# Kernel optimization log

Hardware: AMD Instinct MI355X
Metric: run time of the kernel (lower is better)

The kernel has to match this reference:

```python
import jax, jax.numpy as jnp
import numpy as np

N = 150_000   # total nodes in batched graph
E = 900_000   # total edges (avg in-degree ~ 2*n_gram = 6)
D = 300       # hidden_size_node (GloVe 300d)
B = 512       # number of graphs (docs) in batch
C = 20        # class_num
SLOPE = 0.01  # torch LeakyReLU default negative_slope


def _lrelu(x):
    return jnp.where(x >= 0, x, SLOPE * x)


def setup_inputs() -> dict:
    key = jax.random.key(0)
    ks = jax.random.split(key, 8)
    node_h = jax.random.normal(ks[0], (N, D), dtype=jnp.float32)
    eta = jax.random.uniform(ks[1], (N, 1), dtype=jnp.float32)
    W_attn = jax.random.normal(ks[2], (2 * D, 1), dtype=jnp.float32) * 0.05
    b_attn = jnp.zeros((1,), dtype=jnp.float32)
    W_lin = jax.random.normal(ks[3], (D, C), dtype=jnp.float32) * 0.05
    b_lin = jnp.zeros((C,), dtype=jnp.float32)
    src = jax.random.randint(ks[4], (E,), 0, N, dtype=jnp.int32)
    dst = jax.random.randint(ks[5], (E,), 0, N, dtype=jnp.int32)
    graph_ids = jnp.sort(jax.random.randint(ks[6], (N,), 0, B, dtype=jnp.int32))
    return {
        "node_h": node_h, "eta": eta,
        "W_attn": W_attn, "b_attn": b_attn,
        "W_lin": W_lin, "b_lin": b_lin,
        "src": src, "dst": dst,
        "graph_ids": graph_ids, "num_graphs": B,
    }


def reference(node_h, eta, W_attn, b_attn, W_lin, b_lin, src, dst, graph_ids, num_graphs):
    n = node_h.shape[0]
    # edge_attention: leaky_relu(attn_fc(cat(h_src, h_dst))).
    # cat@W == h_src@W[:D] + h_dst@W[D:], so project per-node first (avoids [E,2D] cat).
    ps = node_h @ W_attn[:D]          # [N,1]
    pd = node_h @ W_attn[D:]          # [N,1]
    w = _lrelu(ps[src] + pd[dst] + b_attn)   # [E,1] edge scores

    # segment softmax over each destination node's mailbox
    deg = jax.ops.segment_sum(jnp.ones((w.shape[0], 1), w.dtype), dst, num_segments=n)  # [N,1]
    wmax = jax.ops.segment_max(w, dst, num_segments=n)
    wmax = jnp.where(deg > 0, wmax, 0.0)     # neutralize -inf for isolated nodes
    ew = jnp.exp(w - wmax[dst])              # [E,1]
    denom = jax.ops.segment_sum(ew, dst, num_segments=n)
    a = ew / jnp.where(denom[dst] > 0, denom[dst], 1.0)   # [E,1] softmax weights

    # gcn_reduce: max over weighted messages a * h_src per destination
    am = a * node_h[src]                      # [E,D]
    agg = jax.ops.segment_max(am, dst, num_segments=n)    # [N,D]
    agg = jnp.where(deg > 0, agg, 0.0)

    # gated update: eta*h + (1-eta)*agg; DGL leaves message-less nodes untouched
    h_new = eta * node_h + (1.0 - eta) * agg
    h_new = jnp.where(deg > 0, h_new, node_h)

    # dgl.sum_nodes per graph, dropout (eval: identity), leaky_relu, classifier
    hg = jax.ops.segment_sum(h_new, graph_ids, num_segments=num_graphs)  # [B,D]
    return _lrelu(hg) @ W_lin + b_lin        # [B,C]
```

## Files before the change

kernel.cpp:

```cpp
#include <hip/hip_runtime.h>
#include <math.h>


#define SLOPE 0.01f
#define KNODES 8
#define MAXT 192

__device__ __forceinline__ float lrelu(float x) { return x >= 0.f ? x : SLOPE * x; }

__device__ __forceinline__ float wrsum(float v) {
#pragma unroll
    for (int m = 32; m >= 1; m >>= 1) v += __shfl_xor(v, m, 64);
    return v;
}
__device__ __forceinline__ float wrmax(float v) {
#pragma unroll
    for (int m = 32; m >= 1; m >>= 1) v = fmaxf(v, __shfl_xor(v, m, 64));
    return v;
}

__device__ __forceinline__ void compute_bpre(const unsigned* __restrict__ bsum,
                                             int nT, unsigned* lb) {
    if (threadIdx.x < 64) {
        int l = threadIdx.x;
        unsigned a0 = (3 * l     < nT) ? bsum[3 * l]     : 0u;
        unsigned a1 = (3 * l + 1 < nT) ? bsum[3 * l + 1] : 0u;
        unsigned a2 = (3 * l + 2 < nT) ? bsum[3 * l + 2] : 0u;
        unsigned tot = a0 + a1 + a2, x = tot;
#pragma unroll
        for (int d = 1; d < 64; d <<= 1) {
            unsigned y = __shfl_up(x, d, 64);
            if (l >= d) x += y;
        }
        unsigned excl = x - tot;
        if (3 * l     < nT) lb[3 * l]     = excl;
        if (3 * l + 1 < nT) lb[3 * l + 1] = excl + a0;
        if (3 * l + 2 < nT) lb[3 * l + 2] = excl + a0 + a1;
    }
    __syncthreads();
}

__global__ __launch_bounds__(256) void k_prep(
    const float* __restrict__ H, const float* __restrict__ Wa,
    const int* __restrict__ dst,
    float* __restrict__ ps, float* __restrict__ pd,
    unsigned* __restrict__ deg,
    unsigned* __restrict__ zbase, size_t zn,
    int N, int D, int E, int nb_ps, int nb_hist) {
    int b = blockIdx.x;
    if (b < nb_ps) {
        int wid  = b * 4 + (threadIdx.x >> 6);
        int lane = threadIdx.x & 63;
        if (wid >= N) return;
        const float4* row = (const float4*)(H + (size_t)wid * D);
        const float4* wa0 = (const float4*)Wa;
        const float4* wa1 = (const float4*)(Wa + D);
        int nv = D >> 2;
        float s0 = 0.f, s1 = 0.f;
        for (int v = lane; v < nv; v += 64) {
            float4 h = row[v], a = wa0[v], c = wa1[v];
            s0 += h.x * a.x + h.y * a.y + h.z * a.z + h.w * a.w;
            s1 += h.x * c.x + h.y * c.y + h.z * c.z + h.w * c.w;
        }
        s0 = wrsum(s0);
        s1 = wrsum(s1);
        if (lane == 0) { ps[wid] = s0; pd[wid] = s1; }
    } else if (b < nb_ps + nb_hist) {
        int e = (b - nb_ps) * 256 + threadIdx.x;
        if (e < E) atomicAdd(&deg[dst[e]], 1u);
    } else {
        int    nbz    = gridDim.x - nb_ps - nb_hist;
        size_t i      = (size_t)(b - nb_ps - nb_hist) * 256 + threadIdx.x;
        size_t stride = (size_t)nbz * 256;
        for (; i < zn; i += stride) zbase[i] = 0u;
    }
}

__global__ __launch_bounds__(256) void k_scan1(
    const unsigned* __restrict__ deg, unsigned* __restrict__ loffs,
    unsigned* __restrict__ bsum, int N) {
    __shared__ unsigned wsum[4];
    int t = threadIdx.x, b = blockIdx.x;
    int base = b * 1024 + t * 4;
    unsigned v[4];
#pragma unroll
    for (int j = 0; j < 4; j++) { int i = base + j; v[j] = (i < N) ? deg[i] : 0u; }
    unsigned p0 = v[0], p1 = p0 + v[1], p2 = p1 + v[2];
    unsigned tot = p2 + v[3];
    unsigned x = tot;
    int lane = t & 63, w = t >> 6;
#pragma unroll
    for (int d = 1; d < 64; d <<= 1) { unsigned y = __shfl_up(x, d, 64); if (lane >= d) x += y; }
    if (lane == 63) wsum[w] = x;
    __syncthreads();
    unsigned woff = 0;
    for (int i = 0; i < w; i++) woff += wsum[i];
    unsigned excl = woff + x - tot;
    unsigned o[4] = {excl, excl + p0, excl + p1, excl + p2};
#pragma unroll
    for (int j = 0; j < 4; j++) { int i = base + j; if (i < N) loffs[i] = o[j]; }
    if (t == 255) bsum[b] = excl + tot;
}

__global__ __launch_bounds__(256) void k_scatter(
    const int* __restrict__ src, const int* __restrict__ dst,
    const unsigned* __restrict__ loffs, const unsigned* __restrict__ bsum,
    unsigned* __restrict__ cur, int* __restrict__ ssrc, int E, int nT) {
    __shared__ unsigned lb[MAXT];
    compute_bpre(bsum, nT, lb);
    int e = blockIdx.x * 256 + threadIdx.x;
    if (e >= E) return;
    int d = dst[e];
    unsigned base = loffs[d] + lb[d >> 10];
    unsigned r = atomicAdd(&cur[d], 1u);
    ssrc[base + r] = src[e];
}

__global__ __launch_bounds__(256) void k_fused(
    const float* __restrict__ H, const float* __restrict__ eta,
    const float* __restrict__ ps, const float* __restrict__ pd,
    const float* __restrict__ battn,
    const unsigned* __restrict__ loffs, const unsigned* __restrict__ bsum,
    const int* __restrict__ ssrc, const int* __restrict__ gid,
    float* __restrict__ hg, int N, int D, int E, int nT) {
    __shared__ unsigned lb[MAXT];
    compute_bpre(bsum, nT, lb);

    int wid  = (blockIdx.x * blockDim.x + threadIdx.x) >> 6;
    int lane = threadIdx.x & 63;
    int n0 = wid * KNODES;
    if (n0 >= N) return;
    int n1 = min(n0 + KNODES, N);
    int nv = D >> 2;
    bool q0 = lane < nv;
    bool q1 = (64 + lane) < nv;
    float b0 = battn[0];

    float sx = 0.f, sy = 0.f, sz = 0.f, sw = 0.f;
    float tx = 0.f, ty = 0.f, tz = 0.f, tw = 0.f;
    int curg = gid[n0];

    for (int n = n0; n < n1; ++n) {
        unsigned e0 = loffs[n] + lb[n >> 10];
        unsigned e1 = (n + 1 < N) ? (loffs[n + 1] + lb[(n + 1) >> 10]) : (unsigned)E;
        int degn = (int)(e1 - e0);
        const float4* hrow = (const float4*)(H + (size_t)n * D);
        float4 h0 = {0, 0, 0, 0}, h1 = {0, 0, 0, 0};
        if (q0) h0 = hrow[lane];
        if (q1) h1 = hrow[64 + lane];
        float hx = h0.x, hy = h0.y, hz = h0.z, hw = h0.w;
        float gx = h1.x, gy = h1.y, gz = h1.z, gw = h1.w;
        if (degn > 0) {
            float pdn = pd[n] + b0;
            float ax = -INFINITY, ay = -INFINITY, az = -INFINITY, aw = -INFINITY;
            float bx = -INFINITY, by = -INFINITY, bz = -INFINITY, bw = -INFINITY;
            if (degn <= 64) {
                int   sn_l = (lane < degn) ? ssrc[e0 + lane] : 0;
                float w_l  = (lane < degn) ? lrelu(ps[sn_l] + pdn) : -INFINITY;
                float m    = wrmax(w_l);
                float ex   = (lane < degn) ? expf(w_l - m) : 0.f;
                float s    = wrsum(ex);
                float a_l  = ex * (1.f / s);
                int e = 0;
                for (; e + 3 < degn; e += 4) {
                    float a0s = __shfl(a_l, e, 64),     a1s = __shfl(a_l, e + 1, 64);
                    float a2s = __shfl(a_l, e + 2, 64), a3s = __shfl(a_l, e + 3, 64);
                    int   s0i = __shfl(sn_l, e, 64),     s1i = __shfl(sn_l, e + 1, 64);
                    int   s2i = __shfl(sn_l, e + 2, 64), s3i = __shfl(sn_l, e + 3, 64);
                    const float4* r0 = (const float4*)(H + (size_t)s0i * D);
                    const float4* r1 = (const float4*)(H + (size_t)s1i * D);
                    const float4* r2 = (const float4*)(H + (size_t)s2i * D);
                    const float4* r3 = (const float4*)(H + (size_t)s3i * D);
                    if (q0) {
                        float4 u0 = r0[lane], u1 = r1[lane], u2 = r2[lane], u3 = r3[lane];
                        ax = fmaxf(fmaxf(fmaxf(ax, a0s * u0.x), a1s * u1.x), fmaxf(a2s * u2.x, a3s * u3.x));
                        ay = fmaxf(fmaxf(fmaxf(ay, a0s * u0.y), a1s * u1.y), fmaxf(a2s * u2.y, a3s * u3.y));
                        az = fmaxf(fmaxf(fmaxf(az, a0s * u0.z), a1s * u1.z), fmaxf(a2s * u2.z, a3s * u3.z));
                        aw = fmaxf(fmaxf(fmaxf(aw, a0s * u0.w), a1s * u1.w), fmaxf(a2s * u2.w, a3s * u3.w));
                    }
                    if (q1) {
                        float4 u0 = r0[64 + lane], u1 = r1[64 + lane], u2 = r2[64 + lane], u3 = r3[64 + lane];
                        bx = fmaxf(fmaxf(fmaxf(bx, a0s * u0.x), a1s * u1.x), fmaxf(a2s * u2.x, a3s * u3.x));
                        by = fmaxf(fmaxf(fmaxf(by, a0s * u0.y), a1s * u1.y), fmaxf(a2s * u2.y, a3s * u3.y));
                        bz = fmaxf(fmaxf(fmaxf(bz, a0s * u0.z), a1s * u1.z), fmaxf(a2s * u2.z, a3s * u3.z));
                        bw = fmaxf(fmaxf(fmaxf(bw, a0s * u0.w), a1s * u1.w), fmaxf(a2s * u2.w, a3s * u3.w));
                    }
                }
                for (; e + 1 < degn; e += 2) {
                    float a0s = __shfl(a_l, e, 64), a1s = __shfl(a_l, e + 1, 64);
                    int   s0i = __shfl(sn_l, e, 64), s1i = __shfl(sn_l, e + 1, 64);
                    const float4* r0 = (const float4*)(H + (size_t)s0i * D);
                    const float4* r1 = (const float4*)(H + (size_t)s1i * D);
                    if (q0) {
                        float4 u0 = r0[lane], u1 = r1[lane];
                        ax = fmaxf(fmaxf(ax, a0s * u0.x), a1s * u1.x);
                        ay = fmaxf(fmaxf(ay, a0s * u0.y), a1s * u1.y);
                        az = fmaxf(fmaxf(az, a0s * u0.z), a1s * u1.z);
                        aw = fmaxf(fmaxf(aw, a0s * u0.w), a1s * u1.w);
                    }
                    if (q1) {
                        float4 u0 = r0[64 + lane], u1 = r1[64 + lane];
                        bx = fmaxf(fmaxf(bx, a0s * u0.x), a1s * u1.x);
                        by = fmaxf(fmaxf(by, a0s * u0.y), a1s * u1.y);
                        bz = fmaxf(fmaxf(bz, a0s * u0.z), a1s * u1.z);
                        bw = fmaxf(fmaxf(bw, a0s * u0.w), a1s * u1.w);
                    }
                }
                if (e < degn) {
                    float a  = __shfl(a_l, e, 64);
                    int   sn = __shfl(sn_l, e, 64);
                    const float4* srow = (const float4*)(H + (size_t)sn * D);
                    if (q0) {
                        float4 v0 = srow[lane];
                        ax = fmaxf(ax, a * v0.x); ay = fmaxf(ay, a * v0.y);
                        az = fmaxf(az, a * v0.z); aw = fmaxf(aw, a * v0.w);
                    }
                    if (q1) {
                        float4 v1 = srow[64 + lane];
                        bx = fmaxf(bx, a * v1.x); by = fmaxf(by, a * v1.y);
                        bz = fmaxf(bz, a * v1.z); bw = fmaxf(bw, a * v1.w);
                    }
                }
            } else {
                float mm = -INFINITY;
                for (unsigned e = e0 + lane; e < e1; e += 64)
                    mm = fmaxf(mm, lrelu(ps[ssrc[e]] + pdn));
                float m = wrmax(mm);
                float ssum = 0.f;
                for (unsigned e = e0 + lane; e < e1; e += 64)
                    ssum += expf(lrelu(ps[ssrc[e]] + pdn) - m);
                float s = wrsum(ssum), inv = 1.f / s;
                for (unsigned e = e0; e < e1; ++e) {
                    int sn = ssrc[e];
                    float a = expf(lrelu(ps[sn] + pdn) - m) * inv;
                    const float4* srow = (const float4*)(H + (size_t)sn * D);
                    if (q0) {
                        float4 v0 = srow[lane];
                        ax = fmaxf(ax, a * v0.x); ay = fmaxf(ay, a * v0.y);
                        az = fmaxf(az, a * v0.z); aw = fmaxf(aw, a * v0.w);
                    }
                    if (q1) {
                        float4 v1 = srow[64 + lane];
                        bx = fmaxf(bx, a * v1.x); by = fmaxf(by, a * v1.y);
                        bz = fmaxf(bz, a * v1.z); bw = fmaxf(bw, a * v1.w);
                    }
                }
            }
            float et = eta[n], om = 1.f - et;
            hx = et * h0.x + om * ax; hy = et * h0.y + om * ay;
            hz = et * h0.z + om * az; hw = et * h0.w + om * aw;
            gx = et * h1.x + om * bx; gy = et * h1.y + om * by;
            gz = et * h1.z + om * bz; gw = et * h1.w + om * bw;
        }
        int g = gid[n];
        if (g != curg) {
            float* row = hg + (size_t)curg * D;
            int c = 4 * lane;
            if (q0) {
                atomicAdd(&row[c + 0], sx); atomicAdd(&row[c + 1], sy);
                atomicAdd(&row[c + 2], sz); atomicAdd(&row[c + 3], sw);
            }
            if (q1) {
                int c1 = 4 * (64 + lane);
                atomicAdd(&row[c1 + 0], tx); atomicAdd(&row[c1 + 1], ty);
                atomicAdd(&row[c1 + 2], tz); atomicAdd(&row[c1 + 3], tw);
            }
            sx = sy = sz = sw = tx = ty = tz = tw = 0.f;
            curg = g;
        }
        sx += hx; sy += hy; sz += hz; sw += hw;
        if (q1) { tx += gx; ty += gy; tz += gz; tw += gw; }
    }
    float* row = hg + (size_t)curg * D;
    int c = 4 * lane;
    if (q0) {
        atomicAdd(&row[c + 0], sx); atomicAdd(&row[c + 1], sy);
        atomicAdd(&row[c + 2], sz); atomicAdd(&row[c + 3], sw);
    }
    if (q1) {
        int c1 = 4 * (64 + lane);
        atomicAdd(&row[c1 + 0], tx); atomicAdd(&row[c1 + 1], ty);
        atomicAdd(&row[c1 + 2], tz); atomicAdd(&row[c1 + 3], tw);
    }
}

__global__ __launch_bounds__(64) void k_out(
    const float* __restrict__ hg, const float* __restrict__ Wl,
    const float* __restrict__ bl, float* __restrict__ out,
    int D, int C) {
    int b = blockIdx.x;
    int c = threadIdx.x;
    if (c >= C) return;
    const float* row = hg + (size_t)b * D;
    float acc = 0.f;
    for (int d = 0; d < D; ++d)
        acc += lrelu(row[d]) * Wl[(size_t)d * C + c];
    out[(size_t)b * C + c] = acc + bl[c];
}

extern "C" void kernel_launch(void* const* d_in, const int* in_sizes, int n_in,
                              void* d_out, int out_size, void* d_ws, size_t ws_size,
                              hipStream_t stream) {
    const float* H   = (const float*)d_in[0];
    const float* eta = (const float*)d_in[1];
    const float* Wa  = (const float*)d_in[2];
    const float* ba  = (const float*)d_in[3];
    const float* Wl  = (const float*)d_in[4];
    const float* bl  = (const float*)d_in[5];
    const int*   src = (const int*)d_in[6];
    const int*   dst = (const int*)d_in[7];
    const int*   gid = (const int*)d_in[8];

    const int N = in_sizes[1];
    const int D = in_sizes[2] / 2;
    const int C = in_sizes[5];
    const int E = in_sizes[6];
    const int B = out_size / C;

    char* w = (char*)d_ws;
    float*    ps    = (float*)w;    w += (size_t)N * 4;
    float*    pd    = (float*)w;    w += (size_t)N * 4;
    unsigned* deg   = (unsigned*)w; w += (size_t)N * 4;
    unsigned* cur   = (unsigned*)w; w += (size_t)N * 4;
    float*    hg    = (float*)w;    w += (size_t)B * D * 4;
    unsigned* loffs = (unsigned*)w; w += (size_t)N * 4;
    unsigned* bsum  = (unsigned*)w; w += 256 * 4;
    int*      ssrc  = (int*)w;      w += (size_t)E * 4;

    hipMemsetAsync(deg, 0, (size_t)N * 4, stream);

    const int nT      = (N + 1023) / 1024;
    const int nb_ps   = (N + 3) / 4;
    const int nb_hist = (E + 255) / 256;
    const int nb_zero = 256;
    const size_t zn   = (size_t)N + (size_t)B * D;

    k_prep<<<dim3(nb_ps + nb_hist + nb_zero), dim3(256), 0, stream>>>(
        H, Wa, dst, ps, pd, deg, cur, zn, N, D, E, nb_ps, nb_hist);
    k_scan1<<<dim3(nT), dim3(256), 0, stream>>>(deg, loffs, bsum, N);
    k_scatter<<<dim3((E + 255) / 256), dim3(256), 0, stream>>>(
        src, dst, loffs, bsum, cur, ssrc, E, nT);
    {
        int waves  = (N + KNODES - 1) / KNODES;
        int blocks = (waves + 3) / 4;
        k_fused<<<dim3(blocks), dim3(256), 0, stream>>>(
            H, eta, ps, pd, ba, loffs, bsum, ssrc, gid, hg, N, D, E, nT);
    }
    k_out<<<dim3(B), dim3(64), 0, stream>>>(hg, Wl, bl, (float*)d_out, D, C);
}
```

Measured before the change: 688.1 us.

## Record edge rank during degree histogram, drop second atomic pass and zeroing blocks

The degree histogram now stores each edge's atomic return value as its rank, so the scatter kernel writes directly to the sorted slot without a second atomic counter array. Zeroing of hg moves into one memset that covers deg and hg together (they are now contiguous), replacing the zeroing blocks inside k_prep. The 4-edge unrolled gather loop in the fused kernel is removed, leaving only the 2-edge loop, and k_out splits the D reduction across four waves. This adds an E-sized rank buffer write and read, in exchange for removing E atomics and the cur array.

```diff
diff --git a/kernel.cpp b/kernel.cpp
--- a/kernel.cpp
+++ b/kernel.cpp
@@ -44,9 +44,8 @@
     const float* __restrict__ H, const float* __restrict__ Wa,
     const int* __restrict__ dst,
     float* __restrict__ ps, float* __restrict__ pd,
-    unsigned* __restrict__ deg,
-    unsigned* __restrict__ zbase, size_t zn,
-    int N, int D, int E, int nb_ps, int nb_hist) {
+    unsigned* __restrict__ deg, unsigned* __restrict__ erank,
+    int N, int D, int E, int nb_ps) {
     int b = blockIdx.x;
     if (b < nb_ps) {
         int wid  = b * 4 + (threadIdx.x >> 6);
@@ -65,14 +64,9 @@
         s0 = wrsum(s0);
         s1 = wrsum(s1);
         if (lane == 0) { ps[wid] = s0; pd[wid] = s1; }
-    } else if (b < nb_ps + nb_hist) {
+    } else {
         int e = (b - nb_ps) * 256 + threadIdx.x;
-        if (e < E) atomicAdd(&deg[dst[e]], 1u);
-    } else {
-        int    nbz    = gridDim.x - nb_ps - nb_hist;
-        size_t i      = (size_t)(b - nb_ps - nb_hist) * 256 + threadIdx.x;
-        size_t stride = (size_t)nbz * 256;
-        for (; i < zn; i += stride) zbase[i] = 0u;
+        if (e < E) erank[e] = atomicAdd(&deg[dst[e]], 1u);
     }
 }
 
@@ -105,15 +99,14 @@
 __global__ __launch_bounds__(256) void k_scatter(
     const int* __restrict__ src, const int* __restrict__ dst,
     const unsigned* __restrict__ loffs, const unsigned* __restrict__ bsum,
-    unsigned* __restrict__ cur, int* __restrict__ ssrc, int E, int nT) {
+    const unsigned* __restrict__ erank,
+    int* __restrict__ ssrc, int E, int nT) {
     __shared__ unsigned lb[MAXT];
     compute_bpre(bsum, nT, lb);
     int e = blockIdx.x * 256 + threadIdx.x;
     if (e >= E) return;
     int d = dst[e];
-    unsigned base = loffs[d] + lb[d >> 10];
-    unsigned r = atomicAdd(&cur[d], 1u);
-    ssrc[base + r] = src[e];
+    ssrc[loffs[d] + lb[d >> 10] + erank[e]] = src[e];
 }
 
 __global__ __launch_bounds__(256) void k_fused(
@@ -162,48 +155,26 @@
                 float s    = wrsum(ex);
                 float a_l  = ex * (1.f / s);
                 int e = 0;
-                for (; e + 3 < degn; e += 4) {
-                    float a0s = __shfl(a_l, e, 64),     a1s = __shfl(a_l, e + 1, 64);
-                    float a2s = __shfl(a_l, e + 2, 64), a3s = __shfl(a_l, e + 3, 64);
-                    int   s0i = __shfl(sn_l, e, 64),     s1i = __shfl(sn_l, e + 1, 64);
-                    int   s2i = __shfl(sn_l, e + 2, 64), s3i = __shfl(sn_l, e + 3, 64);
-                    const float4* r0 = (const float4*)(H + (size_t)s0i * D);
-                    const float4* r1 = (const float4*)(H + (size_t)s1i * D);
-                    const float4* r2 = (const float4*)(H + (size_t)s2i * D);
-                    const float4* r3 = (const float4*)(H + (size_t)s3i * D);
-                    if (q0) {
-                        float4 u0 = r0[lane], u1 = r1[lane], u2 = r2[lane], u3 = r3[lane];
-                        ax = fmaxf(fmaxf(fmaxf(ax, a0s * u0.x), a1s * u1.x), fmaxf(a2s * u2.x, a3s * u3.x));
-                        ay = fmaxf(fmaxf(fmaxf(ay, a0s * u0.y), a1s * u1.y), fmaxf(a2s * u2.y, a3s * u3.y));
-                        az = fmaxf(fmaxf(fmaxf(az, a0s * u0.z), a1s * u1.z), fmaxf(a2s * u2.z, a3s * u3.z));
-                        aw = fmaxf(fmaxf(fmaxf(aw, a0s * u0.w), a1s * u1.w), fmaxf(a2s * u2.w, a3s * u3.w));
-                    }
-                    if (q1) {
-                        float4 u0 = r0[64 + lane], u1 = r1[64 + lane], u2 = r2[64 + lane], u3 = r3[64 + lane];
-                        bx = fmaxf(fmaxf(fmaxf(bx, a0s * u0.x), a1s * u1.x), fmaxf(a2s * u2.x, a3s * u3.x));
-                        by = fmaxf(fmaxf(fmaxf(by, a0s * u0.y), a1s * u1.y), fmaxf(a2s * u2.y, a3s * u3.y));
-                        bz = fmaxf(fmaxf(fmaxf(bz, a0s * u0.z), a1s * u1.z), fmaxf(a2s * u2.z, a3s * u3.z));
-                        bw = fmaxf(fmaxf(fmaxf(bw, a0s * u0.w), a1s * u1.w), fmaxf(a2s * u2.w, a3s * u3.w));
-                    }
-                }
                 for (; e + 1 < degn; e += 2) {
                     float a0s = __shfl(a_l, e, 64), a1s = __shfl(a_l, e + 1, 64);
                     int   s0i = __shfl(sn_l, e, 64), s1i = __shfl(sn_l, e + 1, 64);
                     const float4* r0 = (const float4*)(H + (size_t)s0i * D);
                     const float4* r1 = (const float4*)(H + (size_t)s1i * D);
                     if (q0) {
-                        float4 u0 = r0[lane], u1 = r1[lane];
-                        ax = fmaxf(fmaxf(ax, a0s * u0.x), a1s * u1.x);
-                        ay = fmaxf(fmaxf(ay, a0s * u0.y), a1s * u1.y);
-                        az = fmaxf(fmaxf(az, a0s * u0.z), a1s * u1.z);
-                        aw = fmaxf(fmaxf(aw, a0s * u0.w), a1s * u1.w);
+                        float4 u = r0[lane];
+                        float4 v = r1[lane];
+                        ax = fmaxf(fmaxf(ax, a0s * u.x), a1s * v.x);
+                        ay = fmaxf(fmaxf(ay, a0s * u.y), a1s * v.y);
+                        az = fmaxf(fmaxf(az, a0s * u.z), a1s * v.z);
+                        aw = fmaxf(fmaxf(aw, a0s * u.w), a1s * v.w);
                     }
                     if (q1) {
-                        float4 u0 = r0[64 + lane], u1 = r1[64 + lane];
-                        bx = fmaxf(fmaxf(bx, a0s * u0.x), a1s * u1.x);
-                        by = fmaxf(fmaxf(by, a0s * u0.y), a1s * u1.y);
-                        bz = fmaxf(fmaxf(bz, a0s * u0.z), a1s * u1.z);
-                        bw = fmaxf(fmaxf(bw, a0s * u0.w), a1s * u1.w);
+                        float4 u = r0[64 + lane];
+                        float4 v = r1[64 + lane];
+                        bx = fmaxf(fmaxf(bx, a0s * u.x), a1s * v.x);
+                        by = fmaxf(fmaxf(by, a0s * u.y), a1s * v.y);
+                        bz = fmaxf(fmaxf(bz, a0s * u.z), a1s * v.z);
+                        bw = fmaxf(fmaxf(bw, a0s * u.w), a1s * v.w);
                     }
                 }
                 if (e < degn) {
@@ -284,18 +255,25 @@
     }
 }
 
-__global__ __launch_bounds__(64) void k_out(
+__global__ __launch_bounds__(256) void k_out(
     const float* __restrict__ hg, const float* __restrict__ Wl,
     const float* __restrict__ bl, float* __restrict__ out,
     int D, int C) {
+    __shared__ float part[4][64];
     int b = blockIdx.x;
+    int w = threadIdx.x >> 6, l = threadIdx.x & 63;
+    float acc = 0.f;
+    if (l < C) {
+        const float* row = hg + (size_t)b * D;
+        for (int d = w; d < D; d += 4)
+            acc += lrelu(row[d]) * Wl[(size_t)d * C + l];
+        part[w][l] = acc;
+    }
+    __syncthreads();
     int c = threadIdx.x;
-    if (c >= C) return;
-    const float* row = hg + (size_t)b * D;
-    float acc = 0.f;
-    for (int d = 0; d < D; ++d)
-        acc += lrelu(row[d]) * Wl[(size_t)d * C + c];
-    out[(size_t)b * C + c] = acc + bl[c];
+    if (c < C)
+        out[(size_t)b * C + c] =
+            part[0][c] + part[1][c] + part[2][c] + part[3][c] + bl[c];
 }
 
 extern "C" void kernel_launch(void* const* d_in, const int* in_sizes, int n_in,
@@ -321,30 +299,28 @@
     float*    ps    = (float*)w;    w += (size_t)N * 4;
     float*    pd    = (float*)w;    w += (size_t)N * 4;
     unsigned* deg   = (unsigned*)w; w += (size_t)N * 4;
-    unsigned* cur   = (unsigned*)w; w += (size_t)N * 4;
     float*    hg    = (float*)w;    w += (size_t)B * D * 4;
     unsigned* loffs = (unsigned*)w; w += (size_t)N * 4;
     unsigned* bsum  = (unsigned*)w; w += 256 * 4;
     int*      ssrc  = (int*)w;      w += (size_t)E * 4;
-
-    hipMemsetAsync(deg, 0, (size_t)N * 4, stream);
+    unsigned* erank = (unsigned*)w; w += (size_t)E * 4;
+
+    hipMemsetAsync(deg, 0, ((size_t)N + (size_t)B * D) * 4, stream);
 
     const int nT      = (N + 1023) / 1024;
     const int nb_ps   = (N + 3) / 4;
     const int nb_hist = (E + 255) / 256;
-    const int nb_zero = 256;
-    const size_t zn   = (size_t)N + (size_t)B * D;
-
-    k_prep<<<dim3(nb_ps + nb_hist + nb_zero), dim3(256), 0, stream>>>(
-        H, Wa, dst, ps, pd, deg, cur, zn, N, D, E, nb_ps, nb_hist);
+
+    k_prep<<<dim3(nb_ps + nb_hist), dim3(256), 0, stream>>>(
+        H, Wa, dst, ps, pd, deg, erank, N, D, E, nb_ps);
     k_scan1<<<dim3(nT), dim3(256), 0, stream>>>(deg, loffs, bsum, N);
     k_scatter<<<dim3((E + 255) / 256), dim3(256), 0, stream>>>(
-        src, dst, loffs, bsum, cur, ssrc, E, nT);
+        src, dst, loffs, bsum, erank, ssrc, E, nT);
     {
         int waves  = (N + KNODES - 1) / KNODES;
         int blocks = (waves + 3) / 4;
         k_fused<<<dim3(blocks), dim3(256), 0, stream>>>(
             H, eta, ps, pd, ba, loffs, bsum, ssrc, gid, hg, N, D, E, nT);
     }
-    k_out<<<dim3(B), dim3(64), 0, stream>>>(hg, Wl, bl, (float*)d_out, D, C);
-}
+    k_out<<<dim3(B), dim3(256), 0, stream>>>(hg, Wl, bl, (float*)d_out, D, C);
+}
```

Result: faster. 606.9 us (-11.8%).
